# Optimization experiments

Measured on AMD Instinct MI355X. Metric: run time of the kernel, lower is better.

Reference implementation:

```python
import jax, jax.numpy as jnp
import numpy as np

HEADS = 8
DIM_HEAD = 64
SCALE = DIM_HEAD ** -0.5


def setup_inputs() -> dict:
    key = jax.random.key(0)
    k1, k2, k3, k4 = jax.random.split(key, 4)
    b, n, dim = 4, 1024, 512
    inner = HEADS * DIM_HEAD  # 512
    x = jax.random.normal(k1, (b, n, dim), dtype=jnp.float32)
    spd = jax.random.normal(k2, (b, HEADS, n, n), dtype=jnp.float32)
    head_keep = jnp.ones((HEADS,), dtype=jnp.float32)  # deterministic stand-in for binomial head drop
    w_qkv = jax.random.normal(k3, (dim, 3 * inner), dtype=jnp.float32) * (dim ** -0.5)
    w_out = jax.random.normal(k4, (inner, dim), dtype=jnp.float32) * (inner ** -0.5)
    b_out = jnp.zeros((dim,), dtype=jnp.float32)
    return {"x": x, "spd": spd, "head_keep": head_keep, "w_qkv": w_qkv, "w_out": w_out, "b_out": b_out}


def reference(x, spd, head_keep, w_qkv, w_out, b_out):
    b, n, dim = x.shape
    qkv = x @ w_qkv  # [b, n, 3*inner]
    q, k, v = jnp.split(qkv, 3, axis=-1)

    def to_heads(t):  # [b, n, h*d] -> [b, h, n, d]
        return t.reshape(b, n, HEADS, DIM_HEAD).transpose(0, 2, 1, 3)

    q, k, v = to_heads(q), to_heads(k), to_heads(v)
    dots = jnp.einsum('bhid,bhjd->bhij', q, k) * SCALE + spd  # [b, h, n, n]
    attn = jax.nn.softmax(dots, axis=-1)
    # random head drop + rescale: attn * mask * H / sum(keep)
    keep_sum = jnp.sum(head_keep)
    attn = attn * (head_keep[None, :, None, None] * (HEADS / keep_sum))
    out = jnp.einsum('bhij,bhjd->bhid', attn, v)  # [b, h, n, d]
    out = out.transpose(0, 2, 1, 3).reshape(b, n, HEADS * DIM_HEAD)
    return out @ w_out + b_out
```

## Files before the change

kernel.cpp:

```cpp
#include <hip/hip_runtime.h>
#include <math.h>

#define NSEQ   1024
#define HEADS  8
#define DHEAD  64
#define SCALE  0.125f
#define LOG2E  1.4426950408889634f

typedef unsigned int u32;
typedef unsigned short u16;
typedef short short8 __attribute__((ext_vector_type(8)));
typedef __bf16 bf16x2 __attribute__((ext_vector_type(2)));
typedef __bf16 bf16x8 __attribute__((ext_vector_type(8)));
typedef float f32x4  __attribute__((ext_vector_type(4)));
typedef float f32x16 __attribute__((ext_vector_type(16)));

__device__ __forceinline__ u16 f2bf(float f) {
    __bf16 h = (__bf16)f;
    return __builtin_bit_cast(u16, h);
}
__device__ __forceinline__ u32 pk2(float lo, float hi) {
    bf16x2 v; v[0] = (__bf16)lo; v[1] = (__bf16)hi;
    return __builtin_bit_cast(u32, v);
}
__device__ __forceinline__ short8 cvt8(float4 a, float4 b) {
    bf16x8 v;
    v[0] = (__bf16)a.x; v[1] = (__bf16)a.y; v[2] = (__bf16)a.z; v[3] = (__bf16)a.w;
    v[4] = (__bf16)b.x; v[5] = (__bf16)b.y; v[6] = (__bf16)b.z; v[7] = (__bf16)b.w;
    return __builtin_bit_cast(short8, v);
}
__device__ __forceinline__ float exp2_fast(float x) {
#if __has_builtin(__builtin_amdgcn_exp2f)
    return __builtin_amdgcn_exp2f(x);
#else
    return exp2f(x);
#endif
}
__device__ __forceinline__ f32x4 mfma16(short8 a, short8 b, f32x4 c) {
    return __builtin_amdgcn_mfma_f32_16x16x32_bf16(a, b, c, 0, 0, 0);
}
__device__ __forceinline__ f32x16 mfma32(short8 a, short8 b, f32x16 c) {
    return __builtin_amdgcn_mfma_f32_32x32x16_bf16(a, b, c, 0, 0, 0);
}

__global__ __launch_bounds__(256) void prep(const float* __restrict__ wqkv,
                                            const float* __restrict__ wout,
                                            u16* __restrict__ wqkvT,
                                            u16* __restrict__ woutT) {
    __shared__ float T[64][65];
    const int t = threadIdx.x;
    const int bb = blockIdx.x;
    const float* in; u16* outp; int K, N, n0, k0;
    if (bb < 192) {
        in = wqkv; outp = wqkvT; K = 512; N = 1536;
        n0 = (bb % 24) * 64; k0 = (bb / 24) * 64;
    } else {
        int bid = bb - 192;
        in = wout; outp = woutT; K = 512; N = 512;
        n0 = (bid % 8) * 64; k0 = (bid / 8) * 64;
    }
    #pragma unroll
    for (int rep = 0; rep < 4; ++rep) {
        int r = rep * 16 + (t >> 4), c = (t & 15) * 4;
        float4 v = *(const float4*)&in[(size_t)(k0 + r) * N + n0 + c];
        T[r][c + 0] = v.x; T[r][c + 1] = v.y; T[r][c + 2] = v.z; T[r][c + 3] = v.w;
    }
    __syncthreads();
    const int nl = t >> 2, kb = (t & 3) * 16;
    bf16x8 s0, s1;
    #pragma unroll
    for (int e = 0; e < 8; ++e) s0[e] = (__bf16)T[kb + e][nl];
    #pragma unroll
    for (int e = 0; e < 8; ++e) s1[e] = (__bf16)T[kb + 8 + e][nl];
    *(short8*)&outp[(size_t)(n0 + nl) * K + k0 + kb]     = __builtin_bit_cast(short8, s0);
    *(short8*)&outp[(size_t)(n0 + nl) * K + k0 + kb + 8] = __builtin_bit_cast(short8, s1);
}

__global__ __launch_bounds__(256) void gemm_qkv_mfma(const float* __restrict__ x,
                                                     const u16* __restrict__ wT,
                                                     u16* __restrict__ qb,
                                                     u16* __restrict__ kb,
                                                     u16* __restrict__ vT) {
    __shared__ u16 As[128][72];
    __shared__ u16 Bs[64][72];
    const int t = threadIdx.x, lane = t & 63, w = t >> 6;
    const int wm = w >> 1, wn = w & 1;
    const int l15 = lane & 15, l4 = lane >> 4;
    const int bid = blockIdx.x;
    const int swz = (bid & 7) * 96 + (bid >> 3);
    const int j0 = (swz % 24) * 64, i0 = (swz / 24) * 128;
    const int which = j0 / 512;
    const int b = i0 >> 10;

    f32x4 acc[8];
    #pragma unroll
    for (int i = 0; i < 8; ++i) acc[i] = (f32x4){0.f, 0.f, 0.f, 0.f};

    const int arow0 = t >> 2, c16 = (t & 3) * 16;

    float4 rax[8];
    short8 rb2[2];
    #pragma unroll
    for (int rep = 0; rep < 2; ++rep)
        #pragma unroll
        for (int q = 0; q < 4; ++q)
            rax[rep * 4 + q] = *(const float4*)&x[(size_t)(i0 + rep * 64 + arow0) * 512 + c16 + q * 4];
    #pragma unroll
    for (int q = 0; q < 2; ++q)
        rb2[q] = *(const short8*)&wT[(size_t)(j0 + arow0) * 512 + c16 + q * 8];

    for (int kt = 0; kt < 8; ++kt) {
        __syncthreads();
        #pragma unroll
        for (int rep = 0; rep < 2; ++rep) {
            *(short8*)&As[rep * 64 + arow0][c16]     = cvt8(rax[rep * 4 + 0], rax[rep * 4 + 1]);
            *(short8*)&As[rep * 64 + arow0][c16 + 8] = cvt8(rax[rep * 4 + 2], rax[rep * 4 + 3]);
        }
        *(short8*)&Bs[arow0][c16]     = rb2[0];
        *(short8*)&Bs[arow0][c16 + 8] = rb2[1];
        __syncthreads();
        if (kt < 7) {
            int k0 = (kt + 1) * 64;
            #pragma unroll
            for (int rep = 0; rep < 2; ++rep)
                #pragma unroll
                for (int q = 0; q < 4; ++q)
                    rax[rep * 4 + q] = *(const float4*)&x[(size_t)(i0 + rep * 64 + arow0) * 512 + k0 + c16 + q * 4];
            #pragma unroll
            for (int q = 0; q < 2; ++q)
                rb2[q] = *(const short8*)&wT[(size_t)(j0 + arow0) * 512 + k0 + c16 + q * 8];
        }
        #pragma unroll
        for (int ks = 0; ks < 2; ++ks) {
            if (which < 2) {
                short8 af[4], bf[2];
                #pragma unroll
                for (int m = 0; m < 4; ++m)
                    af[m] = *(const short8*)&As[wm * 64 + m * 16 + l15][ks * 32 + l4 * 8];
                #pragma unroll
                for (int n = 0; n < 2; ++n)
                    bf[n] = *(const short8*)&Bs[wn * 32 + n * 16 + l15][ks * 32 + l4 * 8];
                #pragma unroll
                for (int m = 0; m < 4; ++m)
                    #pragma unroll
                    for (int n = 0; n < 2; ++n)
                        acc[m * 2 + n] = mfma16(af[m], bf[n], acc[m * 2 + n]);
            } else {
                short8 af[2], bf[4];
                #pragma unroll
                for (int mj = 0; mj < 2; ++mj)
                    af[mj] = *(const short8*)&Bs[wn * 32 + mj * 16 + l15][ks * 32 + l4 * 8];
                #pragma unroll
                for (int ni = 0; ni < 4; ++ni)
                    bf[ni] = *(const short8*)&As[wm * 64 + ni * 16 + l15][ks * 32 + l4 * 8];
                #pragma unroll
                for (int mj = 0; mj < 2; ++mj)
                    #pragma unroll
                    for (int ni = 0; ni < 4; ++ni)
                        acc[mj * 4 + ni] = mfma16(af[mj], bf[ni], acc[mj * 4 + ni]);
            }
        }
    }

    if (which < 2) {
        u16* dst = (which == 0) ? qb : kb;
        const int h = (j0 & 511) >> 6;
        #pragma unroll
        for (int m = 0; m < 4; ++m)
            #pragma unroll
            for (int n = 0; n < 2; ++n) {
                int d = wn * 32 + n * 16 + l15;
                #pragma unroll
                for (int r = 0; r < 4; ++r) {
                    int tok = i0 + wm * 64 + m * 16 + l4 * 4 + r;
                    dst[(((size_t)(b * HEADS + h)) * NSEQ + (tok & 1023)) * DHEAD + d] =
                        f2bf(acc[m * 2 + n][r]);
                }
            }
    } else {
        const int h = (j0 - 1024) >> 6;
        #pragma unroll
        for (int mj = 0; mj < 2; ++mj)
            #pragma unroll
            for (int ni = 0; ni < 4; ++ni) {
                int tok = i0 + wm * 64 + ni * 16 + l15;
                #pragma unroll
                for (int r = 0; r < 4; ++r) {
                    int d = wn * 32 + mj * 16 + l4 * 4 + r;
                    vT[(((size_t)(b * HEADS + h)) * DHEAD + d) * NSEQ + (tok & 1023)] =
                        f2bf(acc[mj * 4 + ni][r]);
                }
            }
    }
}

__global__ __launch_bounds__(256, 1) void attn_mfma(const u16* __restrict__ qb,
                                                    const u16* __restrict__ kb,
                                                    const u16* __restrict__ vT,
                                                    const float* __restrict__ spd,
                                                    const float* __restrict__ head_keep,
                                                    u16* __restrict__ ab) {
    __shared__ u16 Qs[128][72];
    __shared__ u16 Kd[2][64][72];
    __shared__ u16 Vd[2][64][72];

    const int t = threadIdx.x, lane = t & 63, w = t >> 6;
    const int hi = lane >> 5, li = lane & 31;
    const int bh = blockIdx.y, b = bh >> 3, h = bh & 7;
    const int i0 = blockIdx.x * 128;
    const int irow = i0 + w * 32 + li;

    const u16* qh = qb + (size_t)bh * NSEQ * DHEAD;
    const u16* kh = kb + (size_t)bh * NSEQ * DHEAD;
    const u16* vh = vT + (size_t)bh * DHEAD * NSEQ;
    const float* sp = spd + (size_t)bh * NSEQ * NSEQ + (size_t)irow * NSEQ + hi * 4;

    #pragma unroll
    for (int rep = 0; rep < 4; ++rep) {
        int row = rep * 32 + (t >> 3), c8 = (t & 7) * 8;
        *(short8*)&Qs[row][c8] = *(const short8*)&qh[(size_t)(i0 + row) * DHEAD + c8];
    }

    const int krow = t >> 3, kc8 = (t & 7) * 8;

    short8 rk[2], rv[2];
    float4 spA[8], spB[8];
    #pragma unroll
    for (int rep = 0; rep < 2; ++rep) {
        rk[rep] = *(const short8*)&kh[(size_t)(rep * 32 + krow) * DHEAD + kc8];
        rv[rep] = *(const short8*)&vh[(size_t)(rep * 32 + krow) * NSEQ + kc8];
    }
    #pragma unroll
    for (int e = 0; e < 8; ++e)
        spA[e] = *(const float4*)&sp[(e >> 2) * 32 + (e & 3) * 8];
    #pragma unroll
    for (int rep = 0; rep < 2; ++rep) {
        *(short8*)&Kd[0][rep * 32 + krow][kc8] = rk[rep];
        *(short8*)&Vd[0][rep * 32 + krow][kc8] = rv[rep];
    }
    __syncthreads();

    float m_s = -1e30f, l_s = 0.f;
    f32x16 o0 = {}, o1 = {};
    #pragma unroll
    for (int r = 0; r < 16; ++r) { o0[r] = 0.f; o1[r] = 0.f; }

#define ATTN_STEP(JT, CUR, SPU, SPL)                                          \
    {                                                                         \
        const int jn_ = (JT) + 1;                                             \
        if (jn_ < 16) {                      \
            int j0n = jn_ * 64;                                               \
            _Pragma("unroll")                                                 \
            for (int rep = 0; rep < 2; ++rep) {                               \
                rk[rep] = *(const short8*)&kh[(size_t)(j0n + rep * 32 + krow) * DHEAD + kc8]; \
                rv[rep] = *(const short8*)&vh[(size_t)(rep * 32 + krow) * NSEQ + j0n + kc8];  \
            }                                                                 \
            _Pragma("unroll")                                                 \
            for (int e = 0; e < 8; ++e)                                       \
                SPL[e] = *(const float4*)&sp[j0n + (e >> 2) * 32 + (e & 3) * 8]; \
        }                                                                     \
        f32x16 s2[2];                                                         \
        _Pragma("unroll")                                                     \
        for (int kg = 0; kg < 2; ++kg) {                                      \
            _Pragma("unroll")                                                 \
            for (int r = 0; r < 16; ++r) s2[kg][r] = 0.f;                     \
            _Pragma("unroll")                                                 \
            for (int ds = 0; ds < 4; ++ds) {                                  \
                short8 ak = *(const short8*)&Kd[CUR][kg * 32 + li][ds * 16 + hi * 8]; \
                short8 bq = *(const short8*)&Qs[w * 32 + li][ds * 16 + hi * 8];       \
                s2[kg] = mfma32(ak, bq, s2[kg]);                              \
            }                                                                 \
        }                                                                     \
                          \
        _Pragma("unroll")                                                     \
        for (int kg = 0; kg < 2; ++kg)                                        \
            _Pragma("unroll")                                                 \
            for (int r = 0; r < 16; ++r)                                      \
                s2[kg][r] = fmaf(s2[kg][r], SCALE, SPU[kg * 4 + (r >> 2)][r & 3]) * LOG2E; \
        float mx_[8];                                                         \
        _Pragma("unroll")                                                     \
        for (int r = 0; r < 8; ++r)                                           \
            mx_[r] = fmaxf(fmaxf(s2[0][r], s2[0][r + 8]),                     \
                           fmaxf(s2[1][r], s2[1][r + 8]));                    \
        float m4_[4];                                                         \
        _Pragma("unroll")                                                     \
        for (int r = 0; r < 4; ++r) m4_[r] = fmaxf(mx_[r], mx_[r + 4]);       \
        float pmax = fmaxf(fmaxf(m4_[0], m4_[1]), fmaxf(m4_[2], m4_[3]));     \
        pmax = fmaxf(pmax, __shfl_xor(pmax, 32));                             \
        if (!__all(pmax <= m_s + 12.0f)) {                                    \
            float mnew = fmaxf(m_s, pmax);                                    \
            float fac = exp2_fast(m_s - mnew);                                \
            m_s = mnew;                                                       \
            l_s *= fac;                                                       \
            _Pragma("unroll")                                                 \
            for (int r = 0; r < 16; ++r) {                                    \
                int ip = (r & 3) + 8 * (r >> 2) + 4 * hi;                     \
                float fr = __shfl(fac, ip);                                   \
                o0[r] *= fr; o1[r] *= fr;                                     \
            }                                                                 \
        }                                                                     \
        float sa0 = 0.f, sa1 = 0.f, sa2 = 0.f, sa3 = 0.f;                     \
        _Pragma("unroll")                                                     \
        for (int kg = 0; kg < 2; ++kg)                                        \
            _Pragma("unroll")                                                 \
            for (int r = 0; r < 16; r += 4) {                                 \
                s2[kg][r + 0] = exp2_fast(s2[kg][r + 0] - m_s); sa0 += s2[kg][r + 0]; \
                s2[kg][r + 1] = exp2_fast(s2[kg][r + 1] - m_s); sa1 += s2[kg][r + 1]; \
                s2[kg][r + 2] = exp2_fast(s2[kg][r + 2] - m_s); sa2 += s2[kg][r + 2]; \
                s2[kg][r + 3] = exp2_fast(s2[kg][r + 3] - m_s); sa3 += s2[kg][r + 3]; \
            }                                                                 \
        float rsum = (sa0 + sa1) + (sa2 + sa3);                               \
        rsum += __shfl_xor(rsum, 32);                                         \
        l_s += rsum;                                                          \
        short8 pf[4];                                                         \
        _Pragma("unroll")                                                     \
        for (int ks = 0; ks < 4; ++ks) {                                      \
            int kg_ = ks >> 1, rb_ = (ks & 1) * 8;                            \
            u32 a0 = pk2(s2[kg_][rb_ + 0], s2[kg_][rb_ + 1]);                 \
            u32 a1 = pk2(s2[kg_][rb_ + 2], s2[kg_][rb_ + 3]);                 \
            u32 a2 = pk2(s2[kg_][rb_ + 4], s2[kg_][rb_ + 5]);                 \
            u32 a3 = pk2(s2[kg_][rb_ + 6], s2[kg_][rb_ + 7]);                 \
            u32 x0 = (u32)__shfl_xor((int)a0, 32);                            \
            u32 x1 = (u32)__shfl_xor((int)a1, 32);                            \
            u32 x2 = (u32)__shfl_xor((int)a2, 32);                            \
            u32 x3 = (u32)__shfl_xor((int)a3, 32);                            \
            union { u32 u[4]; short8 v; } c4;                                 \
            c4.u[0] = hi ? x2 : a0;                                           \
            c4.u[1] = hi ? x3 : a1;                                           \
            c4.u[2] = hi ? a2 : x0;                                           \
            c4.u[3] = hi ? a3 : x1;                                           \
            pf[ks] = c4.v;                                                    \
        }                                                                     \
        _Pragma("unroll")                                                     \
        for (int ks = 0; ks < 4; ++ks) {                                      \
            short8 v0f = *(const short8*)&Vd[CUR][li][ks * 16 + hi * 8];      \
            short8 v1f = *(const short8*)&Vd[CUR][32 + li][ks * 16 + hi * 8]; \
            o0 = mfma32(pf[ks], v0f, o0);                                     \
            o1 = mfma32(pf[ks], v1f, o1);                                     \
        }                                                                     \
        if (jn_ < 16) {                  \
            _Pragma("unroll")                                                 \
            for (int rep = 0; rep < 2; ++rep) {                               \
                *(short8*)&Kd[(CUR) ^ 1][rep * 32 + krow][kc8] = rk[rep];     \
                *(short8*)&Vd[(CUR) ^ 1][rep * 32 + krow][kc8] = rv[rep];     \
            }                                                                 \
            __syncthreads();                                                  \
        }                                                                     \
    }

    for (int jt2 = 0; jt2 < 16; jt2 += 2) {
        ATTN_STEP(jt2,     0, spA, spB)
        ATTN_STEP(jt2 + 1, 1, spB, spA)
    }
#undef ATTN_STEP

    float ksum = 0.f;
    #pragma unroll
    for (int i = 0; i < HEADS; ++i) ksum += head_keep[i];
    const float hscale = head_keep[h] * (float)HEADS / ksum;
    const float inv = hscale / l_s;
    #pragma unroll
    for (int r = 0; r < 16; ++r) {
        int ip = (r & 3) + 8 * (r >> 2) + 4 * hi;
        float invr = __shfl(inv, ip);
        int tok = i0 + w * 32 + ip;
        size_t base = ((size_t)(b * NSEQ) + tok) * 512 + h * DHEAD;
        ab[base + li]      = f2bf(o0[r] * invr);
        ab[base + 32 + li] = f2bf(o1[r] * invr);
    }
}

__global__ __launch_bounds__(256) void gemm_out_mfma(const u16* __restrict__ abuf,
                                                     const u16* __restrict__ wT,
                                                     const float* __restrict__ bias,
                                                     float* __restrict__ out) {
    __shared__ u16 As[64][72];
    __shared__ u16 Bs[64][72];
    const int t = threadIdx.x, lane = t & 63, w = t >> 6;
    const int wm = w >> 1, wn = w & 1;
    const int l15 = lane & 15, l4 = lane >> 4;
    const int bid = blockIdx.x;
    const int swz = (bid & 7) * 64 + (bid >> 3);
    const int j0 = (swz % 8) * 64, i0 = (swz / 8) * 64;

    f32x4 acc[2][2];
    #pragma unroll
    for (int m = 0; m < 2; ++m)
        #pragma unroll
        for (int n = 0; n < 2; ++n) acc[m][n] = (f32x4){0.f, 0.f, 0.f, 0.f};

    const int row0 = t >> 2, c16 = (t & 3) * 16;
    short8 rav[2], rbv[2];
    #pragma unroll
    for (int q = 0; q < 2; ++q) {
        rav[q] = *(const short8*)&abuf[(size_t)(i0 + row0) * 512 + c16 + q * 8];
        rbv[q] = *(const short8*)&wT[(size_t)(j0 + row0) * 512 + c16 + q * 8];
    }

    for (int kt = 0; kt < 8; ++kt) {
        __syncthreads();
        #pragma unroll
        for (int q = 0; q < 2; ++q) {
            *(short8*)&As[row0][c16 + q * 8] = rav[q];
            *(short8*)&Bs[row0][c16 + q * 8] = rbv[q];
        }
        __syncthreads();
        if (kt < 7) {
            int k0 = (kt + 1) * 64;
            #pragma unroll
            for (int q = 0; q < 2; ++q) {
                rav[q] = *(const short8*)&abuf[(size_t)(i0 + row0) * 512 + k0 + c16 + q * 8];
                rbv[q] = *(const short8*)&wT[(size_t)(j0 + row0) * 512 + k0 + c16 + q * 8];
            }
        }
        #pragma unroll
        for (int ks = 0; ks < 2; ++ks) {
            short8 af[2], bf[2];
            #pragma unroll
            for (int m = 0; m < 2; ++m)
                af[m] = *(const short8*)&As[wm * 32 + m * 16 + l15][ks * 32 + l4 * 8];
            #pragma unroll
            for (int n = 0; n < 2; ++n)
                bf[n] = *(const short8*)&Bs[wn * 32 + n * 16 + l15][ks * 32 + l4 * 8];
            #pragma unroll
            for (int m = 0; m < 2; ++m)
                #pragma unroll
                for (int n = 0; n < 2; ++n)
                    acc[m][n] = mfma16(af[m], bf[n], acc[m][n]);
        }
    }

    #pragma unroll
    for (int m = 0; m < 2; ++m)
        #pragma unroll
        for (int n = 0; n < 2; ++n) {
            int col = j0 + wn * 32 + n * 16 + l15;
            float bb = bias[col];
            #pragma unroll
            for (int r = 0; r < 4; ++r) {
                int row = i0 + wm * 32 + m * 16 + l4 * 4 + r;
                out[(size_t)row * 512 + col] = acc[m][n][r] + bb;
            }
        }
}

extern "C" void kernel_launch(void* const* d_in, const int* in_sizes, int n_in,
                              void* d_out, int out_size, void* d_ws, size_t ws_size,
                              hipStream_t stream) {
    const float* x         = (const float*)d_in[0];
    const float* spd       = (const float*)d_in[1];
    const float* head_keep = (const float*)d_in[2];
    const float* w_qkv     = (const float*)d_in[3];
    const float* w_out     = (const float*)d_in[4];
    const float* b_out     = (const float*)d_in[5];
    float* out = (float*)d_out;

    char* ws = (char*)d_ws;
    u16* wqkvT  = (u16*)(ws + (4u << 20));
    u16* woutT  = (u16*)(ws + (4u << 20) + 1572864);
    u16* qb     = (u16*)(ws + (6u << 20));
    u16* kb     = (u16*)(ws + (10u << 20));
    u16* vT     = (u16*)(ws + (14u << 20));
    u16* ab     = (u16*)(ws + (18u << 20));

    prep<<<256, 256, 0, stream>>>(w_qkv, w_out, wqkvT, woutT);
    gemm_qkv_mfma<<<768, 256, 0, stream>>>(x, wqkvT, qb, kb, vT);
    attn_mfma<<<dim3(8, 32), 256, 0, stream>>>(qb, kb, vT, spd, head_keep, ab);
    gemm_out_mfma<<<512, 256, 0, stream>>>(ab, woutT, b_out, out);
}
```

Measured before the change: 73.76 us.

## Stage spd bias through LDS as bf16, deepen prefetch, precast x to bf16

The attention kernel now loads the spd bias with coalesced row-major float4 reads, pre-scales it by log2e and stores it as bf16 in a double-buffered LDS tile. Each lane then reads its own scattered bias entries from LDS. Prefetch depth grows to two tiles ahead for K, V and spd, and Q fragments are held in registers instead of shared memory. The grid is flattened and swizzled so neighbouring blocks share a head. Separately, x is converted to bf16 in the prep kernel, so the QKV GEMM reads half the bytes, though x must be written and read back once more. Rounding the bias to bf16 loses some precision, and the extra LDS traffic and register pressure could cost occupancy.

After: 64.10 us. 13.1% less time.

```diff
diff --git a/kernel.cpp b/kernel.cpp
--- a/kernel.cpp
+++ b/kernel.cpp
@@ -23,11 +23,9 @@
     bf16x2 v; v[0] = (__bf16)lo; v[1] = (__bf16)hi;
     return __builtin_bit_cast(u32, v);
 }
-__device__ __forceinline__ short8 cvt8(float4 a, float4 b) {
-    bf16x8 v;
-    v[0] = (__bf16)a.x; v[1] = (__bf16)a.y; v[2] = (__bf16)a.z; v[3] = (__bf16)a.w;
-    v[4] = (__bf16)b.x; v[5] = (__bf16)b.y; v[6] = (__bf16)b.z; v[7] = (__bf16)b.w;
-    return __builtin_bit_cast(short8, v);
+__device__ __forceinline__ float bf2f(u16 b) {
+    u32 u = ((u32)b) << 16;
+    return __builtin_bit_cast(float, u);
 }
 __device__ __forceinline__ float exp2_fast(float x) {
 #if __has_builtin(__builtin_amdgcn_exp2f)
@@ -43,19 +41,32 @@
     return __builtin_amdgcn_mfma_f32_32x32x16_bf16(a, b, c, 0, 0, 0);
 }
 
-__global__ __launch_bounds__(256) void prep(const float* __restrict__ wqkv,
+__global__ __launch_bounds__(256) void prep(const float* __restrict__ x,
+                                            const float* __restrict__ wqkv,
                                             const float* __restrict__ wout,
+                                            u16* __restrict__ x_bf,
                                             u16* __restrict__ wqkvT,
                                             u16* __restrict__ woutT) {
     __shared__ float T[64][65];
     const int t = threadIdx.x;
     const int bb = blockIdx.x;
+    if (bb < 1024) {
+        int i = (bb * 256 + t) * 8;
+        float4 a = *(const float4*)&x[i];
+        float4 b = *(const float4*)&x[i + 4];
+        bf16x8 v;
+        v[0] = (__bf16)a.x; v[1] = (__bf16)a.y; v[2] = (__bf16)a.z; v[3] = (__bf16)a.w;
+        v[4] = (__bf16)b.x; v[5] = (__bf16)b.y; v[6] = (__bf16)b.z; v[7] = (__bf16)b.w;
+        *(short8*)&x_bf[i] = __builtin_bit_cast(short8, v);
+        return;
+    }
     const float* in; u16* outp; int K, N, n0, k0;
-    if (bb < 192) {
+    if (bb < 1216) {
+        int bid = bb - 1024;
         in = wqkv; outp = wqkvT; K = 512; N = 1536;
-        n0 = (bb % 24) * 64; k0 = (bb / 24) * 64;
+        n0 = (bid % 24) * 64; k0 = (bid / 24) * 64;
     } else {
-        int bid = bb - 192;
+        int bid = bb - 1216;
         in = wout; outp = woutT; K = 512; N = 512;
         n0 = (bid % 8) * 64; k0 = (bid / 8) * 64;
     }
@@ -76,7 +87,7 @@
     *(short8*)&outp[(size_t)(n0 + nl) * K + k0 + kb + 8] = __builtin_bit_cast(short8, s1);
 }
 
-__global__ __launch_bounds__(256) void gemm_qkv_mfma(const float* __restrict__ x,
+__global__ __launch_bounds__(256) void gemm_qkv_mfma(const u16* __restrict__ xb,
                                                      const u16* __restrict__ wT,
                                                      u16* __restrict__ qb,
                                                      u16* __restrict__ kb,
@@ -98,13 +109,12 @@
 
     const int arow0 = t >> 2, c16 = (t & 3) * 16;
 
-    float4 rax[8];
-    short8 rb2[2];
+    short8 ra[4], rb2[2];
     #pragma unroll
     for (int rep = 0; rep < 2; ++rep)
         #pragma unroll
-        for (int q = 0; q < 4; ++q)
-            rax[rep * 4 + q] = *(const float4*)&x[(size_t)(i0 + rep * 64 + arow0) * 512 + c16 + q * 4];
+        for (int q = 0; q < 2; ++q)
+            ra[rep * 2 + q] = *(const short8*)&xb[(size_t)(i0 + rep * 64 + arow0) * 512 + c16 + q * 8];
     #pragma unroll
     for (int q = 0; q < 2; ++q)
         rb2[q] = *(const short8*)&wT[(size_t)(j0 + arow0) * 512 + c16 + q * 8];
@@ -112,20 +122,21 @@
     for (int kt = 0; kt < 8; ++kt) {
         __syncthreads();
         #pragma unroll
-        for (int rep = 0; rep < 2; ++rep) {
-            *(short8*)&As[rep * 64 + arow0][c16]     = cvt8(rax[rep * 4 + 0], rax[rep * 4 + 1]);
-            *(short8*)&As[rep * 64 + arow0][c16 + 8] = cvt8(rax[rep * 4 + 2], rax[rep * 4 + 3]);
-        }
-        *(short8*)&Bs[arow0][c16]     = rb2[0];
-        *(short8*)&Bs[arow0][c16 + 8] = rb2[1];
+        for (int rep = 0; rep < 2; ++rep)
+            #pragma unroll
+            for (int q = 0; q < 2; ++q)
+                *(short8*)&As[rep * 64 + arow0][c16 + q * 8] = ra[rep * 2 + q];
+        #pragma unroll
+        for (int q = 0; q < 2; ++q)
+            *(short8*)&Bs[arow0][c16 + q * 8] = rb2[q];
         __syncthreads();
         if (kt < 7) {
             int k0 = (kt + 1) * 64;
             #pragma unroll
             for (int rep = 0; rep < 2; ++rep)
                 #pragma unroll
-                for (int q = 0; q < 4; ++q)
-                    rax[rep * 4 + q] = *(const float4*)&x[(size_t)(i0 + rep * 64 + arow0) * 512 + k0 + c16 + q * 4];
+                for (int q = 0; q < 2; ++q)
+                    ra[rep * 2 + q] = *(const short8*)&xb[(size_t)(i0 + rep * 64 + arow0) * 512 + k0 + c16 + q * 8];
             #pragma unroll
             for (int q = 0; q < 2; ++q)
                 rb2[q] = *(const short8*)&wT[(size_t)(j0 + arow0) * 512 + k0 + c16 + q * 8];
@@ -200,44 +211,69 @@
                                                     const float* __restrict__ spd,
                                                     const float* __restrict__ head_keep,
                                                     u16* __restrict__ ab) {
-    __shared__ u16 Qs[128][72];
     __shared__ u16 Kd[2][64][72];
     __shared__ u16 Vd[2][64][72];
+    __shared__ u16 Sd[2][128][66];
 
     const int t = threadIdx.x, lane = t & 63, w = t >> 6;
     const int hi = lane >> 5, li = lane & 31;
-    const int bh = blockIdx.y, b = bh >> 3, h = bh & 7;
-    const int i0 = blockIdx.x * 128;
-    const int irow = i0 + w * 32 + li;
+    const int bid = blockIdx.x;
+    const int swz = (bid & 7) * 32 + (bid >> 3);
+    const int bh = swz >> 3, it = swz & 7;
+    const int b = bh >> 3, h = bh & 7;
+    const int i0 = it * 128;
 
     const u16* qh = qb + (size_t)bh * NSEQ * DHEAD;
     const u16* kh = kb + (size_t)bh * NSEQ * DHEAD;
     const u16* vh = vT + (size_t)bh * DHEAD * NSEQ;
-    const float* sp = spd + (size_t)bh * NSEQ * NSEQ + (size_t)irow * NSEQ + hi * 4;
-
-    #pragma unroll
-    for (int rep = 0; rep < 4; ++rep) {
-        int row = rep * 32 + (t >> 3), c8 = (t & 7) * 8;
-        *(short8*)&Qs[row][c8] = *(const short8*)&qh[(size_t)(i0 + row) * DHEAD + c8];
-    }
+    const float* sp = spd + (size_t)bh * NSEQ * NSEQ;
+
+    short8 qreg[4];
+    #pragma unroll
+    for (int ds = 0; ds < 4; ++ds)
+        qreg[ds] = *(const short8*)&qh[(size_t)(i0 + w * 32 + li) * DHEAD + ds * 16 + hi * 8];
 
     const int krow = t >> 3, kc8 = (t & 7) * 8;
-
-    short8 rk[2], rv[2];
-    float4 spA[8], spB[8];
+    const int srow = t >> 4, sc = (t & 15) * 4;
+
+    short8 kA[2], vA[2], kB[2], vB[2];
+    float4 sA[8], sB[8];
+
     #pragma unroll
     for (int rep = 0; rep < 2; ++rep) {
-        rk[rep] = *(const short8*)&kh[(size_t)(rep * 32 + krow) * DHEAD + kc8];
-        rv[rep] = *(const short8*)&vh[(size_t)(rep * 32 + krow) * NSEQ + kc8];
-    }
-    #pragma unroll
-    for (int e = 0; e < 8; ++e)
-        spA[e] = *(const float4*)&sp[(e >> 2) * 32 + (e & 3) * 8];
+        kA[rep] = *(const short8*)&kh[(size_t)(rep * 32 + krow) * DHEAD + kc8];
+        vA[rep] = *(const short8*)&vh[(size_t)(rep * 32 + krow) * NSEQ + kc8];
+    }
+    #pragma unroll
+    for (int rep = 0; rep < 8; ++rep)
+        sA[rep] = *(const float4*)&sp[(size_t)(i0 + rep * 16 + srow) * NSEQ + sc];
     #pragma unroll
     for (int rep = 0; rep < 2; ++rep) {
-        *(short8*)&Kd[0][rep * 32 + krow][kc8] = rk[rep];
-        *(short8*)&Vd[0][rep * 32 + krow][kc8] = rv[rep];
-    }
+        *(short8*)&Kd[0][rep * 32 + krow][kc8] = kA[rep];
+        *(short8*)&Vd[0][rep * 32 + krow][kc8] = vA[rep];
+    }
+    #pragma unroll
+    for (int rep = 0; rep < 8; ++rep) {
+        int rrow = rep * 16 + srow;
+        *(u32*)&Sd[0][rrow][sc]     = pk2(sA[rep].x * LOG2E, sA[rep].y * LOG2E);
+        *(u32*)&Sd[0][rrow][sc + 2] = pk2(sA[rep].z * LOG2E, sA[rep].w * LOG2E);
+    }
+    #pragma unroll
+    for (int rep = 0; rep < 2; ++rep) {
+        kB[rep] = *(const short8*)&kh[(size_t)(64 + rep * 32 + krow) * DHEAD + kc8];
+        vB[rep] = *(const short8*)&vh[(size_t)(rep * 32 + krow) * NSEQ + 64 + kc8];
+    }
+    #pragma unroll
+    for (int rep = 0; rep < 8; ++rep)
+        sB[rep] = *(const float4*)&sp[(size_t)(i0 + rep * 16 + srow) * NSEQ + 64 + sc];
+    #pragma unroll
+    for (int rep = 0; rep < 2; ++rep) {
+        kA[rep] = *(const short8*)&kh[(size_t)(128 + rep * 32 + krow) * DHEAD + kc8];
+        vA[rep] = *(const short8*)&vh[(size_t)(rep * 32 + krow) * NSEQ + 128 + kc8];
+    }
+    #pragma unroll
+    for (int rep = 0; rep < 8; ++rep)
+        sA[rep] = *(const float4*)&sp[(size_t)(i0 + rep * 16 + srow) * NSEQ + 128 + sc];
     __syncthreads();
 
     float m_s = -1e30f, l_s = 0.f;
@@ -245,20 +281,9 @@
     #pragma unroll
     for (int r = 0; r < 16; ++r) { o0[r] = 0.f; o1[r] = 0.f; }
 
-#define ATTN_STEP(JT, CUR, SPU, SPL)                                          \
+#define ATTN_STEP(JT, RK, RV, RS)                                             \
     {                                                                         \
-        const int jn_ = (JT) + 1;                                             \
-        if (jn_ < 16) {                      \
-            int j0n = jn_ * 64;                                               \
-            _Pragma("unroll")                                                 \
-            for (int rep = 0; rep < 2; ++rep) {                               \
-                rk[rep] = *(const short8*)&kh[(size_t)(j0n + rep * 32 + krow) * DHEAD + kc8]; \
-                rv[rep] = *(const short8*)&vh[(size_t)(rep * 32 + krow) * NSEQ + j0n + kc8];  \
-            }                                                                 \
-            _Pragma("unroll")                                                 \
-            for (int e = 0; e < 8; ++e)                                       \
-                SPL[e] = *(const float4*)&sp[j0n + (e >> 2) * 32 + (e & 3) * 8]; \
-        }                                                                     \
+        const int cur = (JT) & 1;                                             \
         f32x16 s2[2];                                                         \
         _Pragma("unroll")                                                     \
         for (int kg = 0; kg < 2; ++kg) {                                      \
@@ -266,26 +291,29 @@
             for (int r = 0; r < 16; ++r) s2[kg][r] = 0.f;                     \
             _Pragma("unroll")                                                 \
             for (int ds = 0; ds < 4; ++ds) {                                  \
-                short8 ak = *(const short8*)&Kd[CUR][kg * 32 + li][ds * 16 + hi * 8]; \
-                short8 bq = *(const short8*)&Qs[w * 32 + li][ds * 16 + hi * 8];       \
-                s2[kg] = mfma32(ak, bq, s2[kg]);                              \
+                short8 ak = *(const short8*)&Kd[cur][kg * 32 + li][ds * 16 + hi * 8]; \
+                s2[kg] = mfma32(ak, qreg[ds], s2[kg]);                        \
             }                                                                 \
         }                                                                     \
-                          \
+        float p2[32];                                                         \
         _Pragma("unroll")                                                     \
         for (int kg = 0; kg < 2; ++kg)                                        \
             _Pragma("unroll")                                                 \
-            for (int r = 0; r < 16; ++r)                                      \
-                s2[kg][r] = fmaf(s2[kg][r], SCALE, SPU[kg * 4 + (r >> 2)][r & 3]) * LOG2E; \
-        float mx_[8];                                                         \
-        _Pragma("unroll")                                                     \
-        for (int r = 0; r < 8; ++r)                                           \
-            mx_[r] = fmaxf(fmaxf(s2[0][r], s2[0][r + 8]),                     \
-                           fmaxf(s2[1][r], s2[1][r + 8]));                    \
-        float m4_[4];                                                         \
-        _Pragma("unroll")                                                     \
-        for (int r = 0; r < 4; ++r) m4_[r] = fmaxf(mx_[r], mx_[r + 4]);       \
-        float pmax = fmaxf(fmaxf(m4_[0], m4_[1]), fmaxf(m4_[2], m4_[3]));     \
+            for (int r = 0; r < 16; ++r) {                                    \
+                int key = kg * 32 + (r & 3) + 8 * (r >> 2) + 4 * hi;          \
+                p2[kg * 16 + r] = fmaf(s2[kg][r], SCALE * LOG2E,              \
+                                       bf2f(Sd[cur][w * 32 + li][key]));      \
+            }                                                                 \
+        float m16[16];                                                        \
+        _Pragma("unroll")                                                     \
+        for (int r = 0; r < 16; ++r) m16[r] = fmaxf(p2[r], p2[r + 16]);       \
+        float m8v[8];                                                         \
+        _Pragma("unroll")                                                     \
+        for (int r = 0; r < 8; ++r) m8v[r] = fmaxf(m16[r], m16[r + 8]);       \
+        float m4v[4];                                                         \
+        _Pragma("unroll")                                                     \
+        for (int r = 0; r < 4; ++r) m4v[r] = fmaxf(m8v[r], m8v[r + 4]);       \
+        float pmax = fmaxf(fmaxf(m4v[0], m4v[1]), fmaxf(m4v[2], m4v[3]));     \
         pmax = fmaxf(pmax, __shfl_xor(pmax, 32));                             \
         if (!__all(pmax <= m_s + 12.0f)) {                                    \
             float mnew = fmaxf(m_s, pmax);                                    \
@@ -301,25 +329,23 @@
         }                                                                     \
         float sa0 = 0.f, sa1 = 0.f, sa2 = 0.f, sa3 = 0.f;                     \
         _Pragma("unroll")                                                     \
-        for (int kg = 0; kg < 2; ++kg)                                        \
-            _Pragma("unroll")                                                 \
-            for (int r = 0; r < 16; r += 4) {                                 \
-                s2[kg][r + 0] = exp2_fast(s2[kg][r + 0] - m_s); sa0 += s2[kg][r + 0]; \
-                s2[kg][r + 1] = exp2_fast(s2[kg][r + 1] - m_s); sa1 += s2[kg][r + 1]; \
-                s2[kg][r + 2] = exp2_fast(s2[kg][r + 2] - m_s); sa2 += s2[kg][r + 2]; \
-                s2[kg][r + 3] = exp2_fast(s2[kg][r + 3] - m_s); sa3 += s2[kg][r + 3]; \
-            }                                                                 \
+        for (int r = 0; r < 32; r += 4) {                                     \
+            p2[r + 0] = exp2_fast(p2[r + 0] - m_s); sa0 += p2[r + 0];         \
+            p2[r + 1] = exp2_fast(p2[r + 1] - m_s); sa1 += p2[r + 1];         \
+            p2[r + 2] = exp2_fast(p2[r + 2] - m_s); sa2 += p2[r + 2];         \
+            p2[r + 3] = exp2_fast(p2[r + 3] - m_s); sa3 += p2[r + 3];         \
+        }                                                                     \
         float rsum = (sa0 + sa1) + (sa2 + sa3);                               \
         rsum += __shfl_xor(rsum, 32);                                         \
         l_s += rsum;                                                          \
         short8 pf[4];                                                         \
         _Pragma("unroll")                                                     \
         for (int ks = 0; ks < 4; ++ks) {                                      \
-            int kg_ = ks >> 1, rb_ = (ks & 1) * 8;                            \
-            u32 a0 = pk2(s2[kg_][rb_ + 0], s2[kg_][rb_ + 1]);                 \
-            u32 a1 = pk2(s2[kg_][rb_ + 2], s2[kg_][rb_ + 3]);                 \
-            u32 a2 = pk2(s2[kg_][rb_ + 4], s2[kg_][rb_ + 5]);                 \
-            u32 a3 = pk2(s2[kg_][rb_ + 6], s2[kg_][rb_ + 7]);                 \
+            int rb = (ks >> 1) * 16 + (ks & 1) * 8;                           \
+            u32 a0 = pk2(p2[rb + 0], p2[rb + 1]);                             \
+            u32 a1 = pk2(p2[rb + 2], p2[rb + 3]);                             \
+            u32 a2 = pk2(p2[rb + 4], p2[rb + 5]);                             \
+            u32 a3 = pk2(p2[rb + 6], p2[rb + 7]);                             \
             u32 x0 = (u32)__shfl_xor((int)a0, 32);                            \
             u32 x1 = (u32)__shfl_xor((int)a1, 32);                            \
             u32 x2 = (u32)__shfl_xor((int)a2, 32);                            \
@@ -333,24 +359,42 @@
         }                                                                     \
         _Pragma("unroll")                                                     \
         for (int ks = 0; ks < 4; ++ks) {                                      \
-            short8 v0f = *(const short8*)&Vd[CUR][li][ks * 16 + hi * 8];      \
-            short8 v1f = *(const short8*)&Vd[CUR][32 + li][ks * 16 + hi * 8]; \
+            short8 v0f = *(const short8*)&Vd[cur][li][ks * 16 + hi * 8];      \
+            short8 v1f = *(const short8*)&Vd[cur][32 + li][ks * 16 + hi * 8]; \
             o0 = mfma32(pf[ks], v0f, o0);                                     \
             o1 = mfma32(pf[ks], v1f, o1);                                     \
         }                                                                     \
-        if (jn_ < 16) {                  \
+        if ((JT) < 15) {                                                      \
+            const int nxt = cur ^ 1;                                          \
             _Pragma("unroll")                                                 \
             for (int rep = 0; rep < 2; ++rep) {                               \
-                *(short8*)&Kd[(CUR) ^ 1][rep * 32 + krow][kc8] = rk[rep];     \
-                *(short8*)&Vd[(CUR) ^ 1][rep * 32 + krow][kc8] = rv[rep];     \
+                *(short8*)&Kd[nxt][rep * 32 + krow][kc8] = RK[rep];           \
+                *(short8*)&Vd[nxt][rep * 32 + krow][kc8] = RV[rep];           \
+            }                                                                 \
+            _Pragma("unroll")                                                 \
+            for (int rep = 0; rep < 8; ++rep) {                               \
+                int rrow = rep * 16 + srow;                                   \
+                *(u32*)&Sd[nxt][rrow][sc]     = pk2(RS[rep].x * LOG2E, RS[rep].y * LOG2E); \
+                *(u32*)&Sd[nxt][rrow][sc + 2] = pk2(RS[rep].z * LOG2E, RS[rep].w * LOG2E); \
+            }                                                                 \
+            if ((JT) < 13) {                                                  \
+                int j0n = ((JT) + 3) * 64;                                    \
+                _Pragma("unroll")                                             \
+                for (int rep = 0; rep < 2; ++rep) {                           \
+                    RK[rep] = *(const short8*)&kh[(size_t)(j0n + rep * 32 + krow) * DHEAD + kc8]; \
+                    RV[rep] = *(const short8*)&vh[(size_t)(rep * 32 + krow) * NSEQ + j0n + kc8];  \
+                }                                                             \
+                _Pragma("unroll")                                             \
+                for (int rep = 0; rep < 8; ++rep)                             \
+                    RS[rep] = *(const float4*)&sp[(size_t)(i0 + rep * 16 + srow) * NSEQ + j0n + sc]; \
             }                                                                 \
             __syncthreads();                                                  \
         }                                                                     \
     }
 
     for (int jt2 = 0; jt2 < 16; jt2 += 2) {
-        ATTN_STEP(jt2,     0, spA, spB)
-        ATTN_STEP(jt2 + 1, 1, spB, spA)
+        ATTN_STEP(jt2,     kB, vB, sB)
+        ATTN_STEP(jt2 + 1, kA, vA, sA)
     }
 #undef ATTN_STEP
 
@@ -456,6 +500,7 @@
     float* out = (float*)d_out;
 
     char* ws = (char*)d_ws;
+    u16* x_bf   = (u16*)(ws);
     u16* wqkvT  = (u16*)(ws + (4u << 20));
     u16* woutT  = (u16*)(ws + (4u << 20) + 1572864);
     u16* qb     = (u16*)(ws + (6u << 20));
@@ -463,8 +508,8 @@
     u16* vT     = (u16*)(ws + (14u << 20));
     u16* ab     = (u16*)(ws + (18u << 20));
 
-    prep<<<256, 256, 0, stream>>>(w_qkv, w_out, wqkvT, woutT);
-    gemm_qkv_mfma<<<768, 256, 0, stream>>>(x, wqkvT, qb, kb, vT);
-    attn_mfma<<<dim3(8, 32), 256, 0, stream>>>(qb, kb, vT, spd, head_keep, ab);
+    prep<<<1280, 256, 0, stream>>>(x, w_qkv, w_out, x_bf, wqkvT, woutT);
+    gemm_qkv_mfma<<<768, 256, 0, stream>>>(x_bf, wqkvT, qb, kb, vT);
+    attn_mfma<<<256, 256, 0, stream>>>(qb, kb, vT, spd, head_keep, ab);
     gemm_out_mfma<<<512, 256, 0, stream>>>(ab, woutT, b_out, out);
 }
```
